# Kernel optimization log

Measured on AMD Instinct MI355X. Metric: run time of the kernel, lower is better.

Reference implementation:

```python
import jax, jax.numpy as jnp
import numpy as np

EMBED = 100
BATCH = 4096
NUM_NEG = 256
U, P, W, RP, B, C = 30000, 50000, 100000, 50000, 5000, 1000


def _tab(k, v, e=EMBED):
    r = 0.5 / e
    w = jax.random.uniform(k, (v + 1, e), minval=-r, maxval=r, dtype=jnp.float32)
    return w.at[-1].set(0.0)  # padding row is zeros, as in torch code


def setup_inputs() -> dict:
    key = jax.random.key(0)
    ks = jax.random.split(key, 10)
    inp = {
        'user_emb': _tab(ks[0], U),
        'product_emb': _tab(ks[1], P),
        'word_emb': _tab(ks[2], W),
        'brand_emb': _tab(ks[3], B),
        'category_emb': _tab(ks[4], C),
        'rproduct_emb': _tab(ks[5], RP),
        'rel_vecs': jax.random.uniform(ks[6], (8, EMBED), minval=-0.5 / EMBED, maxval=0.5 / EMBED, dtype=jnp.float32),
        'purchase_bias': jnp.zeros((P + 1,), jnp.float32),
        'mentions_bias': jnp.zeros((W + 1,), jnp.float32),
        'describe_bias': jnp.zeros((W + 1,), jnp.float32),
        'produced_bias': jnp.zeros((B + 1,), jnp.float32),
        'belongs_bias': jnp.zeros((C + 1,), jnp.float32),
        'also_bought_bias': jnp.zeros((RP + 1,), jnp.float32),
        'also_viewed_bias': jnp.zeros((RP + 1,), jnp.float32),
        'together_bias': jnp.zeros((RP + 1,), jnp.float32),
    }
    # batch_idxs columns: (u, p, w, b, c, rp1, rp2, rp3), each in its own vocab range
    col_max = [U, P, W, B, C, RP, RP, RP]
    cols = [jax.random.randint(jax.random.fold_in(ks[7], i), (BATCH,), 0, m) for i, m in enumerate(col_max)]
    inp['batch_idxs'] = jnp.stack(cols, axis=1)
    # deterministic stand-in for torch.multinomial negative sampling, one row per relation
    neg_max = [P, W, W, B, C, RP, RP, RP]
    negs = [jax.random.randint(jax.random.fold_in(ks[8], i), (NUM_NEG,), 0, m) for i, m in enumerate(neg_max)]
    inp['neg_idxs'] = jnp.stack(negs, axis=0)
    return inp


def _neg_loss(head_tab, tail_tab, rvec, bias_tab, h, t, n):
    hv = head_tab[h]                      # [B,E] gather
    ex = hv + rvec                        # [B,E]
    tv = tail_tab[t]                      # [B,E]
    bias = bias_tab[t]                    # [B]
    pos = jnp.sum(ex * tv, axis=-1) + bias  # bmm([B,1,E],[B,E,1]) == rowwise dot
    nv = tail_tab[n]                      # [N,E]
    neg = jnp.einsum('be,ne->bn', ex, nv) + bias[:, None]  # [B,N]
    pos_loss = -jax.nn.log_sigmoid(pos)   # == -log(sigmoid(pos)), stable
    neg_loss = -jax.nn.log_sigmoid(-neg).sum(axis=1)
    return (pos_loss + neg_loss).mean()


def reference(batch_idxs, neg_idxs, user_emb, product_emb, word_emb, brand_emb,
              category_emb, rproduct_emb, rel_vecs, purchase_bias, mentions_bias,
              describe_bias, produced_bias, belongs_bias, also_bought_bias,
              also_viewed_bias, together_bias):
    # (head_tab, tail_tab, bias_tab, head_col, tail_col) per relation, in original order
    rels = [
        (user_emb, product_emb, purchase_bias, 0, 1),
        (user_emb, word_emb, mentions_bias, 0, 2),
        (product_emb, word_emb, describe_bias, 1, 2),
        (product_emb, brand_emb, produced_bias, 1, 3),
        (product_emb, category_emb, belongs_bias, 1, 4),
        (product_emb, rproduct_emb, also_bought_bias, 1, 5),
        (product_emb, rproduct_emb, also_viewed_bias, 1, 6),
        (product_emb, rproduct_emb, together_bias, 1, 7),
    ]
    loss = jnp.float32(0.0)
    for r, (ht, tt, bt, hc, tc) in enumerate(rels):
        loss = loss + _neg_loss(ht, tt, rel_vecs[r], bt,
                                batch_idxs[:, hc], batch_idxs[:, tc], neg_idxs[r])
    return loss
```

## Files before the change

kernel.cpp:

```cpp
#include <hip/hip_runtime.h>


#define EMBED   100
#define BATCH   4096
#define NUM_NEG 256
#define KC      20
#define BM      64
#define BN      128
#define TM      4
#define TN      8

struct RelP {
    const float* head;
    const float* tail;
    const float* bias;
    int hc, tc;
};

struct Params {
    RelP rel[8];
    const float* rel_vecs;
    const int*   batch_idxs;
    const int*   neg_idxs;
    float*       out;
};

__device__ __forceinline__ float softplus_f(float x) {
    float e = __expf(-fabsf(x));
    return fmaxf(x, 0.0f) + __logf(1.0f + e);
}

__device__ __forceinline__ float block_reduce_atomic(float v, float* out) {
#pragma unroll
    for (int off = 32; off > 0; off >>= 1)
        v += __shfl_down(v, off, 64);
    __shared__ float wsum[4];
    const int wid  = threadIdx.x >> 6;
    const int lane = threadIdx.x & 63;
    if (lane == 0) wsum[wid] = v;
    __syncthreads();
    if (threadIdx.x == 0) {
        const float s = (wsum[0] + wsum[1]) + (wsum[2] + wsum[3]);
        atomicAdd(out, s * (1.0f / BATCH));
    }
    return v;
}

__launch_bounds__(256, 4)
__global__ void ke_neg_kernel(Params p) {
    const int bid = blockIdx.x;
    const int r   = bid & 7;
    const int rb  = (bid >> 3) & 63;
    const int nb  = bid >> 9;
    const int tid = threadIdx.x;
    const int tx  = tid & 15;
    const int ty  = tid >> 4;

    __shared__ float As[KC * BM];
    __shared__ float Bs[KC * BN];

    const RelP rp = p.rel[r];

    const int arow0 = tid & 63;
    const int aj0   = tid >> 6;
    const int h0    = p.batch_idxs[(rb * BM + arow0) * 8 + rp.hc];
    const float* aptr0 = rp.head + (size_t)h0 * EMBED + aj0 * 4;
    const float* rvp0  = p.rel_vecs + r * EMBED + aj0 * 4;
    const bool  doA1 = (tid < 320 - 256);
    const int   h1   = doA1 ? p.batch_idxs[(rb * BM + tid) * 8 + rp.hc] : 0;
    const float* aptr1 = rp.head + (size_t)h1 * EMBED + 16;
    const float* rvp1  = p.rel_vecs + r * EMBED + 16;

    const int bneg0 = tid & 127;
    const int bj0   = tid >> 7;
    const int bj1   = bj0 + 2;
    const int n0    = p.neg_idxs[r * NUM_NEG + nb * BN + bneg0];
    const float* bptr0 = rp.tail + (size_t)n0 * EMBED + bj0 * 4;
    const float* bptr1 = rp.tail + (size_t)n0 * EMBED + bj1 * 4;
    const bool  doB2 = (tid < 640 - 512);
    const int   n2   = doB2 ? p.neg_idxs[r * NUM_NEG + nb * BN + tid] : 0;
    const float* bptr2 = rp.tail + (size_t)n2 * EMBED + 16;

    float acc[TM * TN];
#pragma unroll
    for (int i = 0; i < TM * TN; ++i) acc[i] = 0.0f;

#pragma unroll
    for (int kc = 0; kc < EMBED / KC; ++kc) {
        const int k0 = kc * KC;

        {
            const float4 a  = *(const float4*)(aptr0 + k0);
            const float4 rv = *(const float4*)(rvp0 + k0);
            const int kbase = aj0 * 4;
            As[(kbase + 0) * BM + arow0] = a.x + rv.x;
            As[(kbase + 1) * BM + arow0] = a.y + rv.y;
            As[(kbase + 2) * BM + arow0] = a.z + rv.z;
            As[(kbase + 3) * BM + arow0] = a.w + rv.w;
        }
        if (doA1) {
            const float4 a  = *(const float4*)(aptr1 + k0);
            const float4 rv = *(const float4*)(rvp1 + k0);
            As[16 * BM + tid] = a.x + rv.x;
            As[17 * BM + tid] = a.y + rv.y;
            As[18 * BM + tid] = a.z + rv.z;
            As[19 * BM + tid] = a.w + rv.w;
        }
        {
            const float4 b = *(const float4*)(bptr0 + k0);
            const int kbase = bj0 * 4;
            Bs[(kbase + 0) * BN + bneg0] = b.x;
            Bs[(kbase + 1) * BN + bneg0] = b.y;
            Bs[(kbase + 2) * BN + bneg0] = b.z;
            Bs[(kbase + 3) * BN + bneg0] = b.w;
        }
        {
            const float4 b = *(const float4*)(bptr1 + k0);
            const int kbase = bj1 * 4;
            Bs[(kbase + 0) * BN + bneg0] = b.x;
            Bs[(kbase + 1) * BN + bneg0] = b.y;
            Bs[(kbase + 2) * BN + bneg0] = b.z;
            Bs[(kbase + 3) * BN + bneg0] = b.w;
        }
        if (doB2) {
            const float4 b = *(const float4*)(bptr2 + k0);
            Bs[16 * BN + tid] = b.x;
            Bs[17 * BN + tid] = b.y;
            Bs[18 * BN + tid] = b.z;
            Bs[19 * BN + tid] = b.w;
        }
        __syncthreads();

#pragma unroll 4
        for (int k = 0; k < KC; ++k) {
            const float4 a  = *(const float4*)&As[k * BM + tx * TM];
            const float4 b0 = *(const float4*)&Bs[k * BN + ty * TN];
            const float4 b1 = *(const float4*)&Bs[k * BN + ty * TN + 4];
            const float av[4] = {a.x, a.y, a.z, a.w};
            const float bv[8] = {b0.x, b0.y, b0.z, b0.w, b1.x, b1.y, b1.z, b1.w};
#pragma unroll
            for (int i = 0; i < TM; ++i)
#pragma unroll
                for (int n = 0; n < TN; ++n)
                    acc[i * TN + n] = fmaf(av[i], bv[n], acc[i * TN + n]);
        }
        __syncthreads();
    }

    float local = 0.0f;
#pragma unroll
    for (int i = 0; i < TM; ++i) {
        const int grow = rb * BM + tx * TM + i;
        const int t    = p.batch_idxs[grow * 8 + rp.tc];
        const float bias = rp.bias[t];
#pragma unroll
        for (int n = 0; n < TN; ++n)
            local += softplus_f(acc[i * TN + n] + bias);
    }
    block_reduce_atomic(local, p.out);
}

__launch_bounds__(256, 4)
__global__ void ke_pos_kernel(Params p) {
    const int r      = blockIdx.x & 7;
    const int rowblk = blockIdx.x >> 3;
    const int tid    = threadIdx.x;
    const int row    = rowblk * 256 + tid;

    const RelP rp = p.rel[r];
    const int h = p.batch_idxs[row * 8 + rp.hc];
    const int t = p.batch_idxs[row * 8 + rp.tc];

    const float4* __restrict__ hv = (const float4*)(rp.head + (size_t)h * EMBED);
    const float4* __restrict__ rv = (const float4*)(p.rel_vecs + r * EMBED);
    const float4* __restrict__ tv = (const float4*)(rp.tail + (size_t)t * EMBED);

    float d0 = 0.f, d1 = 0.f, d2 = 0.f, d3 = 0.f;
#pragma unroll
    for (int j = 0; j < EMBED / 4; ++j) {
        const float4 a = hv[j];
        const float4 b = rv[j];
        const float4 v = tv[j];
        d0 = fmaf(a.x + b.x, v.x, d0);
        d1 = fmaf(a.y + b.y, v.y, d1);
        d2 = fmaf(a.z + b.z, v.z, d2);
        d3 = fmaf(a.w + b.w, v.w, d3);
    }
    const float pos = ((d0 + d1) + (d2 + d3)) + rp.bias[t];
    block_reduce_atomic(softplus_f(-pos), p.out);
}

extern "C" void kernel_launch(void* const* d_in, const int* in_sizes, int n_in,
                              void* d_out, int out_size, void* d_ws, size_t ws_size,
                              hipStream_t stream) {
    const float* user  = (const float*)d_in[0];
    const float* prod  = (const float*)d_in[1];
    const float* word  = (const float*)d_in[2];
    const float* brand = (const float*)d_in[3];
    const float* cat   = (const float*)d_in[4];
    const float* rprod = (const float*)d_in[5];

    Params p;
    p.rel_vecs   = (const float*)d_in[6];
    p.batch_idxs = (const int*)d_in[15];
    p.neg_idxs   = (const int*)d_in[16];
    p.out        = (float*)d_out;

    p.rel[0] = {user, prod,  (const float*)d_in[7],  0, 1};
    p.rel[1] = {user, word,  (const float*)d_in[8],  0, 2};
    p.rel[2] = {prod, word,  (const float*)d_in[9],  1, 2};
    p.rel[3] = {prod, brand, (const float*)d_in[10], 1, 3};
    p.rel[4] = {prod, cat,   (const float*)d_in[11], 1, 4};
    p.rel[5] = {prod, rprod, (const float*)d_in[12], 1, 5};
    p.rel[6] = {prod, rprod, (const float*)d_in[13], 1, 6};
    p.rel[7] = {prod, rprod, (const float*)d_in[14], 1, 7};

    hipMemsetAsync(d_out, 0, sizeof(float), stream);
    ke_pos_kernel<<<128, 256, 0, stream>>>(p);
    ke_neg_kernel<<<1024, 256, 0, stream>>>(p);
}
```

Before: 178.8 us.

## Fuse positive-loss into negative GEMM kernel with double-buffered shared tiles

Merges the positive-score kernel into the negative-sampling GEMM kernel, so blocks with nb==0 also compute the row-wise positive dot products for their 64 rows. The launch count drops from two kernels to one. The K-loop gains register-prefetched, double-buffered shared memory tiles so global loads overlap compute and one barrier per chunk is removed. The thread tile is remapped from 4x8 to 8x4. The extra buffers double shared memory use, and nb==0 blocks carry extra work, which creates load imbalance.

After: 574.6 us. 3.21x slower.

```diff
diff --git a/kernel.cpp b/kernel.cpp
--- a/kernel.cpp
+++ b/kernel.cpp
@@ -7,8 +7,7 @@
 #define KC      20
 #define BM      64
 #define BN      128
-#define TM      4
-#define TN      8
+#define NCHUNK  5
 
 struct RelP {
     const float* head;
@@ -30,34 +29,18 @@
     return fmaxf(x, 0.0f) + __logf(1.0f + e);
 }
 
-__device__ __forceinline__ float block_reduce_atomic(float v, float* out) {
-#pragma unroll
-    for (int off = 32; off > 0; off >>= 1)
-        v += __shfl_down(v, off, 64);
-    __shared__ float wsum[4];
-    const int wid  = threadIdx.x >> 6;
-    const int lane = threadIdx.x & 63;
-    if (lane == 0) wsum[wid] = v;
-    __syncthreads();
-    if (threadIdx.x == 0) {
-        const float s = (wsum[0] + wsum[1]) + (wsum[2] + wsum[3]);
-        atomicAdd(out, s * (1.0f / BATCH));
-    }
-    return v;
-}
-
 __launch_bounds__(256, 4)
-__global__ void ke_neg_kernel(Params p) {
+__global__ void ke_kernel(Params p) {
     const int bid = blockIdx.x;
     const int r   = bid & 7;
     const int rb  = (bid >> 3) & 63;
     const int nb  = bid >> 9;
     const int tid = threadIdx.x;
-    const int tx  = tid & 15;
-    const int ty  = tid >> 4;
-
-    __shared__ float As[KC * BM];
-    __shared__ float Bs[KC * BN];
+    const int tx  = tid & 7;
+    const int ty  = tid >> 3;
+
+    __shared__ float As[2][KC * BM];
+    __shared__ float Bs[2][KC * BN];
 
     const RelP rp = p.rel[r];
 
@@ -66,128 +49,148 @@
     const int h0    = p.batch_idxs[(rb * BM + arow0) * 8 + rp.hc];
     const float* aptr0 = rp.head + (size_t)h0 * EMBED + aj0 * 4;
     const float* rvp0  = p.rel_vecs + r * EMBED + aj0 * 4;
-    const bool  doA1 = (tid < 320 - 256);
+    const bool  doA1 = (tid < 64);
     const int   h1   = doA1 ? p.batch_idxs[(rb * BM + tid) * 8 + rp.hc] : 0;
     const float* aptr1 = rp.head + (size_t)h1 * EMBED + 16;
     const float* rvp1  = p.rel_vecs + r * EMBED + 16;
 
     const int bneg0 = tid & 127;
     const int bj0   = tid >> 7;
-    const int bj1   = bj0 + 2;
     const int n0    = p.neg_idxs[r * NUM_NEG + nb * BN + bneg0];
     const float* bptr0 = rp.tail + (size_t)n0 * EMBED + bj0 * 4;
-    const float* bptr1 = rp.tail + (size_t)n0 * EMBED + bj1 * 4;
-    const bool  doB2 = (tid < 640 - 512);
+    const float* bptr1 = bptr0 + 8;
+    const bool  doB2 = (tid < 128);
     const int   n2   = doB2 ? p.neg_idxs[r * NUM_NEG + nb * BN + tid] : 0;
     const float* bptr2 = rp.tail + (size_t)n2 * EMBED + 16;
 
-    float acc[TM * TN];
-#pragma unroll
-    for (int i = 0; i < TM * TN; ++i) acc[i] = 0.0f;
-
-#pragma unroll
-    for (int kc = 0; kc < EMBED / KC; ++kc) {
+    float acc[8][4];
+#pragma unroll
+    for (int i = 0; i < 8; ++i)
+#pragma unroll
+        for (int n = 0; n < 4; ++n) acc[i][n] = 0.0f;
+
+    float4 pa0, prv0, pa1, prv1, pb0, pb1, pb2;
+
+    auto load_chunk = [&](int kc) {
         const int k0 = kc * KC;
-
+        pa0  = *(const float4*)(aptr0 + k0);
+        prv0 = *(const float4*)(rvp0 + k0);
+        if (doA1) { pa1 = *(const float4*)(aptr1 + k0); prv1 = *(const float4*)(rvp1 + k0); }
+        pb0 = *(const float4*)(bptr0 + k0);
+        pb1 = *(const float4*)(bptr1 + k0);
+        if (doB2) pb2 = *(const float4*)(bptr2 + k0);
+    };
+
+    auto write_buf = [&](int b) {
         {
-            const float4 a  = *(const float4*)(aptr0 + k0);
-            const float4 rv = *(const float4*)(rvp0 + k0);
-            const int kbase = aj0 * 4;
-            As[(kbase + 0) * BM + arow0] = a.x + rv.x;
-            As[(kbase + 1) * BM + arow0] = a.y + rv.y;
-            As[(kbase + 2) * BM + arow0] = a.z + rv.z;
-            As[(kbase + 3) * BM + arow0] = a.w + rv.w;
+            const int kb = aj0 * 4;
+            As[b][(kb + 0) * BM + arow0] = pa0.x + prv0.x;
+            As[b][(kb + 1) * BM + arow0] = pa0.y + prv0.y;
+            As[b][(kb + 2) * BM + arow0] = pa0.z + prv0.z;
+            As[b][(kb + 3) * BM + arow0] = pa0.w + prv0.w;
         }
         if (doA1) {
-            const float4 a  = *(const float4*)(aptr1 + k0);
-            const float4 rv = *(const float4*)(rvp1 + k0);
-            As[16 * BM + tid] = a.x + rv.x;
-            As[17 * BM + tid] = a.y + rv.y;
-            As[18 * BM + tid] = a.z + rv.z;
-            As[19 * BM + tid] = a.w + rv.w;
+            As[b][16 * BM + tid] = pa1.x + prv1.x;
+            As[b][17 * BM + tid] = pa1.y + prv1.y;
+            As[b][18 * BM + tid] = pa1.z + prv1.z;
+            As[b][19 * BM + tid] = pa1.w + prv1.w;
         }
         {
-            const float4 b = *(const float4*)(bptr0 + k0);
-            const int kbase = bj0 * 4;
-            Bs[(kbase + 0) * BN + bneg0] = b.x;
-            Bs[(kbase + 1) * BN + bneg0] = b.y;
-            Bs[(kbase + 2) * BN + bneg0] = b.z;
-            Bs[(kbase + 3) * BN + bneg0] = b.w;
+            const int kb = bj0 * 4;
+            Bs[b][(kb + 0) * BN + bneg0] = pb0.x;
+            Bs[b][(kb + 1) * BN + bneg0] = pb0.y;
+            Bs[b][(kb + 2) * BN + bneg0] = pb0.z;
+            Bs[b][(kb + 3) * BN + bneg0] = pb0.w;
         }
         {
-            const float4 b = *(const float4*)(bptr1 + k0);
-            const int kbase = bj1 * 4;
-            Bs[(kbase + 0) * BN + bneg0] = b.x;
-            Bs[(kbase + 1) * BN + bneg0] = b.y;
-            Bs[(kbase + 2) * BN + bneg0] = b.z;
-            Bs[(kbase + 3) * BN + bneg0] = b.w;
+            const int kb = bj0 * 4 + 8;
+            Bs[b][(kb + 0) * BN + bneg0] = pb1.x;
+            Bs[b][(kb + 1) * BN + bneg0] = pb1.y;
+            Bs[b][(kb + 2) * BN + bneg0] = pb1.z;
+            Bs[b][(kb + 3) * BN + bneg0] = pb1.w;
         }
         if (doB2) {
-            const float4 b = *(const float4*)(bptr2 + k0);
-            Bs[16 * BN + tid] = b.x;
-            Bs[17 * BN + tid] = b.y;
-            Bs[18 * BN + tid] = b.z;
-            Bs[19 * BN + tid] = b.w;
-        }
-        __syncthreads();
-
-#pragma unroll 4
+            Bs[b][16 * BN + tid] = pb2.x;
+            Bs[b][17 * BN + tid] = pb2.y;
+            Bs[b][18 * BN + tid] = pb2.z;
+            Bs[b][19 * BN + tid] = pb2.w;
+        }
+    };
+
+    auto compute = [&](int b) {
+#pragma unroll
         for (int k = 0; k < KC; ++k) {
-            const float4 a  = *(const float4*)&As[k * BM + tx * TM];
-            const float4 b0 = *(const float4*)&Bs[k * BN + ty * TN];
-            const float4 b1 = *(const float4*)&Bs[k * BN + ty * TN + 4];
-            const float av[4] = {a.x, a.y, a.z, a.w};
-            const float bv[8] = {b0.x, b0.y, b0.z, b0.w, b1.x, b1.y, b1.z, b1.w};
-#pragma unroll
-            for (int i = 0; i < TM; ++i)
-#pragma unroll
-                for (int n = 0; n < TN; ++n)
-                    acc[i * TN + n] = fmaf(av[i], bv[n], acc[i * TN + n]);
-        }
-        __syncthreads();
+            const float4 a0 = *(const float4*)&As[b][k * BM + tx * 8];
+            const float4 a1 = *(const float4*)&As[b][k * BM + tx * 8 + 4];
+            const float4 bv = *(const float4*)&Bs[b][k * BN + ty * 4];
+            const float av[8] = {a0.x, a0.y, a0.z, a0.w, a1.x, a1.y, a1.z, a1.w};
+            const float bw[4] = {bv.x, bv.y, bv.z, bv.w};
+#pragma unroll
+            for (int i = 0; i < 8; ++i)
+#pragma unroll
+                for (int n = 0; n < 4; ++n)
+                    acc[i][n] = fmaf(av[i], bw[n], acc[i][n]);
+        }
+    };
+
+    load_chunk(0);
+    write_buf(0);
+    __syncthreads();
+#pragma unroll
+    for (int kc = 0; kc < NCHUNK; ++kc) {
+        if (kc + 1 < NCHUNK) load_chunk(kc + 1);
+        compute(kc & 1);
+        if (kc + 1 < NCHUNK) {
+            write_buf((kc + 1) & 1);
+            __syncthreads();
+        }
     }
 
     float local = 0.0f;
 #pragma unroll
-    for (int i = 0; i < TM; ++i) {
-        const int grow = rb * BM + tx * TM + i;
+    for (int i = 0; i < 8; ++i) {
+        const int grow = rb * BM + tx * 8 + i;
         const int t    = p.batch_idxs[grow * 8 + rp.tc];
         const float bias = rp.bias[t];
 #pragma unroll
-        for (int n = 0; n < TN; ++n)
-            local += softplus_f(acc[i * TN + n] + bias);
-    }
-    block_reduce_atomic(local, p.out);
-}
-
-__launch_bounds__(256, 4)
-__global__ void ke_pos_kernel(Params p) {
-    const int r      = blockIdx.x & 7;
-    const int rowblk = blockIdx.x >> 3;
-    const int tid    = threadIdx.x;
-    const int row    = rowblk * 256 + tid;
-
-    const RelP rp = p.rel[r];
-    const int h = p.batch_idxs[row * 8 + rp.hc];
-    const int t = p.batch_idxs[row * 8 + rp.tc];
-
-    const float4* __restrict__ hv = (const float4*)(rp.head + (size_t)h * EMBED);
-    const float4* __restrict__ rv = (const float4*)(p.rel_vecs + r * EMBED);
-    const float4* __restrict__ tv = (const float4*)(rp.tail + (size_t)t * EMBED);
-
-    float d0 = 0.f, d1 = 0.f, d2 = 0.f, d3 = 0.f;
-#pragma unroll
-    for (int j = 0; j < EMBED / 4; ++j) {
-        const float4 a = hv[j];
-        const float4 b = rv[j];
-        const float4 v = tv[j];
-        d0 = fmaf(a.x + b.x, v.x, d0);
-        d1 = fmaf(a.y + b.y, v.y, d1);
-        d2 = fmaf(a.z + b.z, v.z, d2);
-        d3 = fmaf(a.w + b.w, v.w, d3);
-    }
-    const float pos = ((d0 + d1) + (d2 + d3)) + rp.bias[t];
-    block_reduce_atomic(softplus_f(-pos), p.out);
+        for (int n = 0; n < 4; ++n)
+            local += softplus_f(acc[i][n] + bias);
+    }
+
+    if (nb == 0 && tid < BM) {
+        const int row = rb * BM + tid;
+        const int h = p.batch_idxs[row * 8 + rp.hc];
+        const int t = p.batch_idxs[row * 8 + rp.tc];
+        const float4* __restrict__ hv  = (const float4*)(rp.head + (size_t)h * EMBED);
+        const float4* __restrict__ rv4 = (const float4*)(p.rel_vecs + r * EMBED);
+        const float4* __restrict__ tv  = (const float4*)(rp.tail + (size_t)t * EMBED);
+        float d0 = 0.f, d1 = 0.f, d2 = 0.f, d3 = 0.f;
+#pragma unroll
+        for (int j = 0; j < EMBED / 4; ++j) {
+            const float4 a = hv[j];
+            const float4 b = rv4[j];
+            const float4 v = tv[j];
+            d0 = fmaf(a.x + b.x, v.x, d0);
+            d1 = fmaf(a.y + b.y, v.y, d1);
+            d2 = fmaf(a.z + b.z, v.z, d2);
+            d3 = fmaf(a.w + b.w, v.w, d3);
+        }
+        const float pos = ((d0 + d1) + (d2 + d3)) + rp.bias[t];
+        local += softplus_f(-pos);
+    }
+
+#pragma unroll
+    for (int off = 32; off > 0; off >>= 1)
+        local += __shfl_down(local, off, 64);
+    __shared__ float wsum[4];
+    const int wid  = tid >> 6;
+    const int lane = tid & 63;
+    if (lane == 0) wsum[wid] = local;
+    __syncthreads();
+    if (tid == 0) {
+        const float s = (wsum[0] + wsum[1]) + (wsum[2] + wsum[3]);
+        atomicAdd(p.out, s * (1.0f / BATCH));
+    }
 }
 
 extern "C" void kernel_launch(void* const* d_in, const int* in_sizes, int n_in,
@@ -216,6 +219,5 @@
     p.rel[7] = {prod, rprod, (const float*)d_in[14], 1, 7};
 
     hipMemsetAsync(d_out, 0, sizeof(float), stream);
-    ke_pos_kernel<<<128, 256, 0, stream>>>(p);
-    ke_neg_kernel<<<1024, 256, 0, stream>>>(p);
+    ke_kernel<<<1024, 256, 0, stream>>>(p);
 }
```
